# Kernel tuning notes

Hardware: AMD Instinct MI355X
Metric: run time of the kernel (lower is better)

## Reference

```python
import jax, jax.numpy as jnp
import numpy as np

B, N, D, S = 128, 1024, 512, 64
ITERS = 3
EPS = 1e-8


def setup_inputs() -> dict:
    key = jax.random.key(0)
    ks = jax.random.split(key, 10)
    inp = {
        "inputs_pe": jax.random.normal(ks[0], (B, N, D), dtype=jnp.float32),
        "inputs": jax.random.normal(ks[1], (B, N, D), dtype=jnp.float32),
        "slots": jax.random.normal(ks[2], (1, S, D), dtype=jnp.float32),
        "W1": jax.random.normal(ks[3], (D, D), dtype=jnp.float32) * 0.02,
        "b1": jnp.zeros((D,), dtype=jnp.float32),
        "W2": jax.random.normal(ks[4], (D, D), dtype=jnp.float32) * 0.02,
        "b2": jnp.zeros((D,), dtype=jnp.float32),
        "W3": jax.random.normal(ks[5], (D, D), dtype=jnp.float32) * 0.02,
        "b3": jnp.zeros((D,), dtype=jnp.float32),
    }
    return inp


def reference(inputs_pe, inputs, slots, W1, b1, W2, b2, W3, b3):
    b = inputs_pe.shape[0]
    scale = D ** (-0.5)
    # to_k: Linear -> ReLU -> Linear -> ReLU -> Linear (torch Linear: x @ W.T + b)
    h = jax.nn.relu(jnp.einsum('bnd,ed->bne', inputs_pe, W1) + b1)
    h = jax.nn.relu(jnp.einsum('bnd,ed->bne', h, W2) + b2)
    k = jnp.einsum('bnd,ed->bne', h, W3) + b3  # [b, n, d]

    q = jnp.broadcast_to(slots, (b, S, D))  # slots never updated in the loop
    for _ in range(ITERS):
        dots = jnp.einsum('bid,bjd->bij', q, k) * scale  # [b, S, n]
        s_j = dots.sum(axis=2, keepdims=True)            # sum over keys j -> [b, S, 1]
        s_all = dots.sum(axis=(1, 2), keepdims=True)     # total per batch -> [b, 1, 1]
        dots = dots / s_j * s_all
        attn = jax.nn.sigmoid(dots)
        attn2 = attn / (attn.sum(axis=-1, keepdims=True) + EPS)
        updates = jnp.einsum('bjd,bij->bid', inputs, attn2)  # [b, S, d]
    return updates, attn
```

## Files before the change

kernel.cpp:

```cpp
#include <hip/hip_runtime.h>
#include <stdint.h>

#define Bb 128
#define Nn 1024
#define Dd 512
#define Ss 64

constexpr float kScale = 0.044194173824159216f;
constexpr float kEps = 1e-8f;

typedef __bf16 bf16x8 __attribute__((ext_vector_type(8)));
typedef float f32x4 __attribute__((ext_vector_type(4)));
typedef float f32x16 __attribute__((ext_vector_type(16)));
typedef unsigned short ushort8 __attribute__((ext_vector_type(8)));

#define MFMA32 __builtin_amdgcn_mfma_f32_32x32x16_bf16

__device__ inline unsigned short f2bf_rne(float x) {
  unsigned u = __builtin_bit_cast(unsigned, x);
  u += 0x7FFFu + ((u >> 16) & 1u);
  return (unsigned short)(u >> 16);
}
__device__ inline float bf2f(unsigned short h) {
  unsigned u = ((unsigned)h) << 16;
  return __builtin_bit_cast(float, u);
}

__device__ inline void gl_lds16(const void* g, void* l) {
  typedef unsigned int u32;
  auto gp = (u32 __attribute__((address_space(1)))*)(unsigned long long)(uintptr_t)g;
  auto lp = (u32 __attribute__((address_space(3)))*)(unsigned int)(uintptr_t)l;
  __builtin_amdgcn_global_load_lds(gp, lp, 16, 0, 0);
}

__global__ void cast_split_i(const float* __restrict__ in,
                             unsigned short* __restrict__ out, int n8) {
  int i = blockIdx.x * blockDim.x + threadIdx.x;
  const int stride = gridDim.x * blockDim.x;
  for (; i < n8; i += stride) {
    const float4 v0 = ((const float4*)in)[i * 2];
    const float4 v1 = ((const float4*)in)[i * 2 + 1];
    float f[8] = {v0.x, v0.y, v0.z, v0.w, v1.x, v1.y, v1.z, v1.w};
    ushort8 h, lo;
#pragma unroll
    for (int j = 0; j < 8; j++) {
      h[j] = f2bf_rne(f[j]);
      lo[j] = f2bf_rne(f[j] - bf2f(h[j]));
    }
    ((ushort8*)out)[i * 2] = h;
    ((ushort8*)out)[i * 2 + 1] = lo;
  }
}

template <int ACT>
__global__ __launch_bounds__(512, 1) void gemm_g2(
    const unsigned short* __restrict__ A, const unsigned short* __restrict__ W,
    const float* __restrict__ bias, unsigned short* __restrict__ C) {
  constexpr int NS = 16;
  extern __shared__ unsigned short lds[];
  const int t = threadIdx.x, l = t & 63, w = t >> 6;
  const int wr = w >> 2, wc = w & 3;

  const int wg = ((blockIdx.x & 7) << 7) + (blockIdx.x >> 3);
  const long rowA0 = (long)(wg >> 1) * 256;
  const int colB0 = (wg & 1) * 256;

  const unsigned short* base8 = (w < 4) ? A + rowA0 * 1024 : W + (long)colB0 * 1024;
  const int qs = (l & 7) ^ ((l >> 3) & 7);
  const unsigned short* srcp[8];
  int dstp[8];
#pragma unroll
  for (int j = 0; j < 8; j++) {
    const int cl = (w & 3) * 8 + j;
    const int row = cl * 8 + (l >> 3);
    srcp[j] = base8 + (long)row * 1024 + qs * 8;
    dstp[j] = (w < 4 ? 0 : 16384) + cl * 512;
  }
#define STG(s)                                                            \
  {                                                                       \
    unsigned short* bq_ = lds + ((s) & 1) * 32768;                        \
    _Pragma("unroll") for (int j = 0; j < 8; j++)                         \
        gl_lds16(srcp[j] + (s) * 64, bq_ + dstp[j]);                      \
  }

  const int p0 = ((2 * (l >> 5)) ^ (l & 7)) * 8;
  int aoff[4], boff[2];
#pragma unroll
  for (int m = 0; m < 4; m++) aoff[m] = (wr * 128 + m * 32 + (l & 31)) * 64 + p0;
#pragma unroll
  for (int n = 0; n < 2; n++) boff[n] = 16384 + (wc * 64 + n * 32 + (l & 31)) * 64 + p0;

  f32x16 acc[4][2] = {};
  bf16x8 ah[4], al[4], bh0, bl0, bh1, bl1;

#define PH()                                                              \
  __builtin_amdgcn_s_barrier();                                           \
  asm volatile("s_waitcnt lgkmcnt(0)" ::: "memory");                      \
  __builtin_amdgcn_sched_barrier(0);

#define M6(MI, BH, BL, NI)                                                \
  __builtin_amdgcn_s_setprio(1);                                          \
  acc[MI][NI] = MFMA32(ah[MI], BH, acc[MI][NI], 0, 0, 0);                 \
  acc[MI][NI] = MFMA32(al[MI], BH, acc[MI][NI], 0, 0, 0);                 \
  acc[MI][NI] = MFMA32(ah[MI], BL, acc[MI][NI], 0, 0, 0);                 \
  acc[MI + 1][NI] = MFMA32(ah[MI + 1], BH, acc[MI + 1][NI], 0, 0, 0);     \
  acc[MI + 1][NI] = MFMA32(al[MI + 1], BH, acc[MI + 1][NI], 0, 0, 0);     \
  acc[MI + 1][NI] = MFMA32(ah[MI + 1], BL, acc[MI + 1][NI], 0, 0, 0);     \
  __builtin_amdgcn_s_setprio(0);                                          \
  __builtin_amdgcn_sched_barrier(0);

  STG(0);

  for (int s = 0; s < NS; ++s) {
    asm volatile("s_waitcnt vmcnt(0)" ::: "memory");
    __builtin_amdgcn_s_barrier();
    __builtin_amdgcn_sched_barrier(0);
    if (s + 1 < NS) STG(s + 1);
    const unsigned short* bq = lds + (s & 1) * 32768;

    ah[0] = *(const bf16x8*)(bq + aoff[0]);
    al[0] = *(const bf16x8*)(bq + (aoff[0] ^ 8));
    ah[1] = *(const bf16x8*)(bq + aoff[1]);
    al[1] = *(const bf16x8*)(bq + (aoff[1] ^ 8));
    bh0 = *(const bf16x8*)(bq + boff[0]);
    bl0 = *(const bf16x8*)(bq + (boff[0] ^ 8));
    PH()
    M6(0, bh0, bl0, 0)
    ah[2] = *(const bf16x8*)(bq + aoff[2]);
    al[2] = *(const bf16x8*)(bq + (aoff[2] ^ 8));
    ah[3] = *(const bf16x8*)(bq + aoff[3]);
    al[3] = *(const bf16x8*)(bq + (aoff[3] ^ 8));
    PH()
    M6(2, bh0, bl0, 0)
    bh1 = *(const bf16x8*)(bq + boff[1]);
    bl1 = *(const bf16x8*)(bq + (boff[1] ^ 8));
    PH()
    M6(0, bh1, bl1, 1)
    ah[0] = *(const bf16x8*)(bq + (aoff[0] ^ 32));
    al[0] = *(const bf16x8*)(bq + (aoff[0] ^ 40));
    ah[1] = *(const bf16x8*)(bq + (aoff[1] ^ 32));
    al[1] = *(const bf16x8*)(bq + (aoff[1] ^ 40));
    bh0 = *(const bf16x8*)(bq + (boff[0] ^ 32));
    bl0 = *(const bf16x8*)(bq + (boff[0] ^ 40));
    PH()
    M6(2, bh1, bl1, 1)
    ah[2] = *(const bf16x8*)(bq + (aoff[2] ^ 32));
    al[2] = *(const bf16x8*)(bq + (aoff[2] ^ 40));
    ah[3] = *(const bf16x8*)(bq + (aoff[3] ^ 32));
    al[3] = *(const bf16x8*)(bq + (aoff[3] ^ 40));
    PH()
    M6(0, bh0, bl0, 0)
    bh1 = *(const bf16x8*)(bq + (boff[1] ^ 32));
    bl1 = *(const bf16x8*)(bq + (boff[1] ^ 40));
    PH()
    M6(2, bh0, bl0, 0)
    PH()
    M6(0, bh1, bl1, 1)
    M6(2, bh1, bl1, 1)
  }
#undef STG
#undef PH
#undef M6

#pragma unroll
  for (int m = 0; m < 4; m++)
#pragma unroll
    for (int n = 0; n < 2; n++) {
      const int col = colB0 + wc * 64 + n * 32 + (l & 31);
      const float bv = bias[col];
      const int cofs = (col >> 3) * 16 + (col & 7);
#pragma unroll
      for (int r = 0; r < 16; r++) {
        const long row = rowA0 + wr * 128 + m * 32 + (r & 3) + 8 * (r >> 2) + 4 * (l >> 5);
        float xv = acc[m][n][r] + bv;
        if (ACT) xv = fmaxf(xv, 0.0f);
        const unsigned short h = f2bf_rne(xv);
        unsigned short* cp = C + row * 1024 + cofs;
        cp[0] = h;
        cp[8] = f2bf_rne(xv - bf2f(h));
      }
    }
}

__global__ __launch_bounds__(256) void gemm_dots_split(
    const unsigned short* __restrict__ QI, const unsigned short* __restrict__ KI,
    float* __restrict__ dots) {
  constexpr int K = 512, BM = 64, BN = 128, BK = 32;
  __shared__ __align__(16) unsigned short lah[BM * BK];
  __shared__ __align__(16) unsigned short lal[BM * BK];
  __shared__ __align__(16) unsigned short lbh[BN * BK];
  __shared__ __align__(16) unsigned short lbl[BN * BK];
  const int t = threadIdx.x, l = t & 63, w = t >> 6;
  const int b = blockIdx.x >> 3, bc = blockIdx.x & 7;
  const unsigned short* kb = KI + (long)b * Nn * 1024;
  f32x4 acc[4][2] = {};

  const int qbase = (t >> 2) * 1024 + (t & 3) * 16;
  const long kbase0 = (long)(bc * BN + (t >> 2)) * 1024 + (t & 3) * 16;
  const long kbase1 = (long)(bc * BN + 64 + (t >> 2)) * 1024 + (t & 3) * 16;

  for (int k0 = 0; k0 < K; k0 += BK) {
    const int ko = k0 * 2;
    const int lo = w * 512;
    gl_lds16(QI + qbase + ko, lah + lo);
    gl_lds16(QI + qbase + ko + 8, lal + lo);
    gl_lds16(kb + kbase0 + ko, lbh + lo);
    gl_lds16(kb + kbase0 + ko + 8, lbl + lo);
    gl_lds16(kb + kbase1 + ko, lbh + 2048 + lo);
    gl_lds16(kb + kbase1 + ko + 8, lbl + 2048 + lo);
    __syncthreads();
    bf16x8 ah[4], al[4], bh[2], bl[2];
#pragma unroll
    for (int m = 0; m < 4; m++) {
      const int off = (m * 16 + (l & 15)) * BK + (l >> 4) * 8;
      ah[m] = *(const bf16x8*)(lah + off);
      al[m] = *(const bf16x8*)(lal + off);
    }
#pragma unroll
    for (int n = 0; n < 2; n++) {
      const int off = (w * 32 + n * 16 + (l & 15)) * BK + (l >> 4) * 8;
      bh[n] = *(const bf16x8*)(lbh + off);
      bl[n] = *(const bf16x8*)(lbl + off);
    }
#pragma unroll
    for (int m = 0; m < 4; m++)
#pragma unroll
      for (int n = 0; n < 2; n++) {
        acc[m][n] = __builtin_amdgcn_mfma_f32_16x16x32_bf16(ah[m], bh[n], acc[m][n], 0, 0, 0);
        acc[m][n] = __builtin_amdgcn_mfma_f32_16x16x32_bf16(al[m], bh[n], acc[m][n], 0, 0, 0);
        acc[m][n] = __builtin_amdgcn_mfma_f32_16x16x32_bf16(ah[m], bl[n], acc[m][n], 0, 0, 0);
      }
    __syncthreads();
  }
  float* dp = dots + (long)b * Ss * Nn;
#pragma unroll
  for (int m = 0; m < 4; m++) {
    const int row = m * 16 + (l >> 4) * 4;
#pragma unroll
    for (int n = 0; n < 2; n++) {
      const int col = bc * BN + w * 32 + n * 16 + (l & 15);
#pragma unroll
      for (int r = 0; r < 4; r++) dp[(long)(row + r) * Nn + col] = acc[m][n][r] * kScale;
    }
  }
}

__global__ __launch_bounds__(256) void reduce_k(
    const float* __restrict__ dots, float* __restrict__ s_j, float* __restrict__ s_all) {
  const int b = blockIdx.x, t = threadIdx.x, l = t & 63, w = t >> 6;
  const float4* dp = (const float4*)(dots + (long)b * Ss * Nn);
  __shared__ float rowacc[64][4];
  __shared__ float rowsum[64];
  for (int r = 0; r < 64; ++r) {
    const float4 v = dp[r * 256 + t];
    float s = v.x + v.y + v.z + v.w;
#pragma unroll
    for (int off = 32; off; off >>= 1) s += __shfl_down(s, off);
    if (l == 0) rowacc[r][w] = s;
  }
  __syncthreads();
  if (t < 64) {
    const float v = rowacc[t][0] + rowacc[t][1] + rowacc[t][2] + rowacc[t][3];
    rowsum[t] = v;
    s_j[b * 64 + t] = v;
  }
  __syncthreads();
  if (t < 64) {
    float v = rowsum[t];
#pragma unroll
    for (int off = 32; off; off >>= 1) v += __shfl_down(v, off);
    if (t == 0) s_all[b] = v;
  }
}

__global__ __launch_bounds__(256) void attn_k(
    const float* __restrict__ dots, const float* __restrict__ s_j,
    const float* __restrict__ s_all, float* __restrict__ attn_out,
    float* __restrict__ inv_r) {
  const int bi = blockIdx.x;
  const int b = bi >> 6;
  const int t = threadIdx.x;
  const float ratio = s_all[b] / s_j[bi];
  const float* dp = dots + (long)bi * Nn;
  float* ap = attn_out + (long)bi * Nn;
  float s = 0.f;
#pragma unroll
  for (int qq = 0; qq < 4; qq++) {
    const int j = qq * 256 + t;
    const float x = dp[j] * ratio;
    const float a = 1.f / (1.f + expf(-x));
    ap[j] = a;
    s += a;
  }
  __shared__ float red[256];
  red[t] = s;
  __syncthreads();
  for (int off = 128; off > 0; off >>= 1) {
    if (t < off) red[t] += red[t + off];
    __syncthreads();
  }
  if (t == 0) inv_r[bi] = 1.f / (red[0] + kEps);
}

__global__ __launch_bounds__(256) void updates_k6(
    const float* __restrict__ attn, const float* __restrict__ inputs,
    const float* __restrict__ inv_r, float* __restrict__ out0) {
  constexpr int NT2 = 32;
  constexpr int BUF_F = 6144;
  extern __shared__ float ldsf[];
  const int t = threadIdx.x, l = t & 63, w = t >> 6;
  const int b = blockIdx.x >> 2, dt = blockIdx.x & 3;
  const int ig = t >> 5, dg = t & 31;
  const float* inb = inputs + (size_t)b * (Nn * Dd) + dt * 128;
  const float* attsrc = attn + (size_t)b * (Ss * Nn) + (size_t)(t >> 2) * Nn + (t & 3) * 8;
  float acc[8][4] = {};
  float4 ga0, ga1, gb0, gb1;

#define UISSUE(bufi, tile, G0, G1)                                        \
  {                                                                       \
    const int j0_ = (tile)*32;                                            \
    G0 = *(const float4*)(attsrc + j0_);                                  \
    G1 = *(const float4*)(attsrc + j0_ + 4);                              \
    float* db_ = ldsf + (bufi)*BUF_F;                                     \
    _Pragma("unroll") for (int i_ = 0; i_ < 4; i_++) {                    \
      const int row_ = i_ * 8 + w * 2 + (l >> 5);                         \
      gl_lds16(inb + (size_t)(j0_ + row_) * Dd + (l & 31) * 4,            \
               db_ + (i_ * 8 + w * 2) * 128);                             \
    }                                                                     \
  }

#define UWRITE(bufi, G0, G1)                                              \
  {                                                                       \
    float* ab_ = ldsf + (bufi)*BUF_F + 4096;                              \
    const int col_ = t >> 2;                                              \
    const int r0_ = (t & 3) * 8;                                          \
    ab_[(r0_ + 0) * 64 + col_] = G0.x;                                    \
    ab_[(r0_ + 1) * 64 + col_] = G0.y;                                    \
    ab_[(r0_ + 2) * 64 + col_] = G0.z;                                    \
    ab_[(r0_ + 3) * 64 + col_] = G0.w;                                    \
    ab_[(r0_ + 4) * 64 + col_] = G1.x;                                    \
    ab_[(r0_ + 5) * 64 + col_] = G1.y;                                    \
    ab_[(r0_ + 6) * 64 + col_] = G1.z;                                    \
    ab_[(r0_ + 7) * 64 + col_] = G1.w;                                    \
  }

#define UCOMP(bufi)                                                       \
  {                                                                       \
    const float* db_ = ldsf + (bufi)*BUF_F;                               \
    const float* ab_ = db_ + 4096;                                        \
    _Pragma("unroll 4") for (int jj = 0; jj < 32; jj++) {                 \
      float av[8];                                                        \
      float4 vv;                                                          \
      *(float4*)&av[0] = *(const float4*)(ab_ + jj * 64 + ig * 8);        \
      *(float4*)&av[4] = *(const float4*)(ab_ + jj * 64 + ig * 8 + 4);    \
      vv = *(const float4*)(db_ + jj * 128 + dg * 4);                     \
      _Pragma("unroll") for (int m_ = 0; m_ < 8; m_++) {                  \
        acc[m_][0] = __builtin_fmaf(av[m_], vv.x, acc[m_][0]);            \
        acc[m_][1] = __builtin_fmaf(av[m_], vv.y, acc[m_][1]);            \
        acc[m_][2] = __builtin_fmaf(av[m_], vv.z, acc[m_][2]);            \
        acc[m_][3] = __builtin_fmaf(av[m_], vv.w, acc[m_][3]);            \
      }                                                                   \
    }                                                                     \
  }

  UISSUE(0, 0, ga0, ga1);
  UISSUE(1, 1, gb0, gb1);
  UWRITE(0, ga0, ga1);

  for (int tt = 0; tt < NT2; tt += 2) {
    asm volatile("s_waitcnt vmcnt(6)" ::: "memory");
    UWRITE((tt + 1) % 3, gb0, gb1);
    asm volatile("s_waitcnt lgkmcnt(0)" ::: "memory");
    __builtin_amdgcn_s_barrier();
    __builtin_amdgcn_sched_barrier(0);
    if (tt < NT2 - 2) UISSUE((tt + 2) % 3, tt + 2, ga0, ga1);
    UCOMP(tt % 3);
    if (tt + 1 < NT2 - 1) {
      asm volatile("s_waitcnt vmcnt(6)" ::: "memory");
    } else {
      asm volatile("s_waitcnt vmcnt(0)" ::: "memory");
    }
    if (tt + 1 < NT2 - 1) UWRITE((tt + 2) % 3, ga0, ga1);
    asm volatile("s_waitcnt lgkmcnt(0)" ::: "memory");
    __builtin_amdgcn_s_barrier();
    __builtin_amdgcn_sched_barrier(0);
    if (tt + 1 < NT2 - 2) UISSUE((tt + 3) % 3, tt + 3, gb0, gb1);
    UCOMP((tt + 1) % 3);
  }
#undef UISSUE
#undef UWRITE
#undef UCOMP

#pragma unroll
  for (int m = 0; m < 8; m++) {
    const int i = ig * 8 + m;
    const float ir = inv_r[b * 64 + i];
    float4 o;
    o.x = acc[m][0] * ir; o.y = acc[m][1] * ir; o.z = acc[m][2] * ir; o.w = acc[m][3] * ir;
    float* op = out0 + (size_t)(b * 64 + i) * Dd + dt * 128 + dg * 4;
    *(float4*)op = o;
  }
}

extern "C" void kernel_launch(void* const* d_in, const int* in_sizes, int n_in,
                              void* d_out, int out_size, void* d_ws, size_t ws_size,
                              hipStream_t stream) {
  (void)in_sizes; (void)n_in; (void)out_size; (void)ws_size;
  const float* inputs_pe = (const float*)d_in[0];
  const float* inputs = (const float*)d_in[1];
  const float* slots = (const float*)d_in[2];
  const float* W1 = (const float*)d_in[3];
  const float* b1 = (const float*)d_in[4];
  const float* W2 = (const float*)d_in[5];
  const float* b2 = (const float*)d_in[6];
  const float* W3 = (const float*)d_in[7];
  const float* b3 = (const float*)d_in[8];

  char* ws = (char*)d_ws;
  size_t off = 0;
  auto alloc = [&](size_t bytes) -> void* {
    void* p = ws + off;
    off += (bytes + 255) & ~(size_t)255;
    return p;
  };
  const size_t actB = (size_t)Bb * Nn * 1024 * 2;
  unsigned short* AI = (unsigned short*)alloc(actB);
  unsigned short* BI = (unsigned short*)alloc(actB);
  unsigned short* w1i = (unsigned short*)alloc(Dd * 1024 * 2);
  unsigned short* w2i = (unsigned short*)alloc(Dd * 1024 * 2);
  unsigned short* w3i = (unsigned short*)alloc(Dd * 1024 * 2);
  unsigned short* qi = (unsigned short*)alloc(Ss * 1024 * 2);
  float* dotsb = (float*)alloc((size_t)Bb * Ss * Nn * 4);
  float* s_j = (float*)alloc(Bb * Ss * 4);
  float* s_all = (float*)alloc(Bb * 4);
  float* inv_r = (float*)alloc(Bb * Ss * 4);

  float* out_updates = (float*)d_out;
  float* out_attn = out_updates + (size_t)Bb * Ss * Dd;

  const int kLdsG = 2 * 64 * 1024;
  const int kLdsU = 3 * 24 * 1024;
  hipFuncSetAttribute(reinterpret_cast<const void*>(gemm_g2<1>),
                      hipFuncAttributeMaxDynamicSharedMemorySize, kLdsG);
  hipFuncSetAttribute(reinterpret_cast<const void*>(gemm_g2<0>),
                      hipFuncAttributeMaxDynamicSharedMemorySize, kLdsG);
  hipFuncSetAttribute(reinterpret_cast<const void*>(updates_k6),
                      hipFuncAttributeMaxDynamicSharedMemorySize, kLdsU);

  cast_split_i<<<4096, 256, 0, stream>>>(inputs_pe, AI, Bb * Nn * Dd / 8);
  cast_split_i<<<128, 256, 0, stream>>>(W1, w1i, Dd * Dd / 8);
  cast_split_i<<<128, 256, 0, stream>>>(W2, w2i, Dd * Dd / 8);
  cast_split_i<<<128, 256, 0, stream>>>(W3, w3i, Dd * Dd / 8);
  cast_split_i<<<16, 256, 0, stream>>>(slots, qi, Ss * Dd / 8);

  gemm_g2<1><<<1024, 512, kLdsG, stream>>>(AI, w1i, b1, BI);
  gemm_g2<1><<<1024, 512, kLdsG, stream>>>(BI, w2i, b2, AI);
  gemm_g2<0><<<1024, 512, kLdsG, stream>>>(AI, w3i, b3, BI);

  gemm_dots_split<<<Bb * 8, 256, 0, stream>>>(qi, BI, dotsb);
  reduce_k<<<Bb, 256, 0, stream>>>(dotsb, s_j, s_all);
  attn_k<<<Bb * Ss, 256, 0, stream>>>(dotsb, s_j, s_all, out_attn, inv_r);
  updates_k6<<<Bb * 4, 256, kLdsU, stream>>>(out_attn, inputs, inv_r, out_updates);
}
```

Measured before the change: 1.022 ms.

## Double-buffer dots GEMM loads and fuse row-sum reduction with sigmoid attention

The dots GEMM now uses a two-slot dynamic LDS buffer, so the next K-tile's global-to-LDS copies are issued while the current tile runs on the MFMAs, with one barrier per step instead of two. The separate reduce and attention kernels are merged into one kernel per batch. It computes row sums and the total, then applies sigmoid and per-row normalisation in a second pass, which removes a launch and the s_j and s_all intermediates. In exchange the fused kernel runs only 128 blocks, which may underuse the GPU compared with the old 8192-block attention launch, and the dots kernel uses more LDS.

Result: slower. 1.056 ms (+3.4%).

```diff
diff --git a/kernel.cpp b/kernel.cpp
--- a/kernel.cpp
+++ b/kernel.cpp
@@ -182,45 +182,56 @@
     }
 }
 
-__global__ __launch_bounds__(256) void gemm_dots_split(
+__global__ __launch_bounds__(256) void gemm_dots2(
     const unsigned short* __restrict__ QI, const unsigned short* __restrict__ KI,
     float* __restrict__ dots) {
-  constexpr int K = 512, BM = 64, BN = 128, BK = 32;
-  __shared__ __align__(16) unsigned short lah[BM * BK];
-  __shared__ __align__(16) unsigned short lal[BM * BK];
-  __shared__ __align__(16) unsigned short lbh[BN * BK];
-  __shared__ __align__(16) unsigned short lbl[BN * BK];
+  constexpr int NS = 16;
+  constexpr int SLOT = 12288;
+  extern __shared__ unsigned short ldsd[];
   const int t = threadIdx.x, l = t & 63, w = t >> 6;
   const int b = blockIdx.x >> 3, bc = blockIdx.x & 7;
   const unsigned short* kb = KI + (long)b * Nn * 1024;
   f32x4 acc[4][2] = {};
 
   const int qbase = (t >> 2) * 1024 + (t & 3) * 16;
-  const long kbase0 = (long)(bc * BN + (t >> 2)) * 1024 + (t & 3) * 16;
-  const long kbase1 = (long)(bc * BN + 64 + (t >> 2)) * 1024 + (t & 3) * 16;
-
-  for (int k0 = 0; k0 < K; k0 += BK) {
-    const int ko = k0 * 2;
-    const int lo = w * 512;
-    gl_lds16(QI + qbase + ko, lah + lo);
-    gl_lds16(QI + qbase + ko + 8, lal + lo);
-    gl_lds16(kb + kbase0 + ko, lbh + lo);
-    gl_lds16(kb + kbase0 + ko + 8, lbl + lo);
-    gl_lds16(kb + kbase1 + ko, lbh + 2048 + lo);
-    gl_lds16(kb + kbase1 + ko + 8, lbl + 2048 + lo);
-    __syncthreads();
+  const long kbase0 = (long)(bc * 128 + (t >> 2)) * 1024 + (t & 3) * 16;
+  const long kbase1 = (long)(bc * 128 + 64 + (t >> 2)) * 1024 + (t & 3) * 16;
+  const int lo = w * 512;
+
+#define DSTG(s)                                                           \
+  {                                                                       \
+    unsigned short* bq_ = ldsd + ((s) & 1) * SLOT;                        \
+    const int ko_ = (s) * 64;                                             \
+    gl_lds16(QI + qbase + ko_, bq_ + lo);                                 \
+    gl_lds16(QI + qbase + ko_ + 8, bq_ + 2048 + lo);                      \
+    gl_lds16(kb + kbase0 + ko_, bq_ + 4096 + lo);                         \
+    gl_lds16(kb + kbase0 + ko_ + 8, bq_ + 8192 + lo);                     \
+    gl_lds16(kb + kbase1 + ko_, bq_ + 4096 + 2048 + lo);                  \
+    gl_lds16(kb + kbase1 + ko_ + 8, bq_ + 8192 + 2048 + lo);              \
+  }
+
+  DSTG(0);
+
+  for (int s = 0; s < NS; ++s) {
+    asm volatile("s_waitcnt lgkmcnt(0)" ::: "memory");
+    asm volatile("s_waitcnt vmcnt(0)" ::: "memory");
+    __builtin_amdgcn_s_barrier();
+    __builtin_amdgcn_sched_barrier(0);
+    if (s + 1 < NS) DSTG(s + 1);
+    const unsigned short* bq = ldsd + (s & 1) * SLOT;
+
     bf16x8 ah[4], al[4], bh[2], bl[2];
 #pragma unroll
     for (int m = 0; m < 4; m++) {
-      const int off = (m * 16 + (l & 15)) * BK + (l >> 4) * 8;
-      ah[m] = *(const bf16x8*)(lah + off);
-      al[m] = *(const bf16x8*)(lal + off);
+      const int off = (m * 16 + (l & 15)) * 32 + (l >> 4) * 8;
+      ah[m] = *(const bf16x8*)(bq + off);
+      al[m] = *(const bf16x8*)(bq + 2048 + off);
     }
 #pragma unroll
     for (int n = 0; n < 2; n++) {
-      const int off = (w * 32 + n * 16 + (l & 15)) * BK + (l >> 4) * 8;
-      bh[n] = *(const bf16x8*)(lbh + off);
-      bl[n] = *(const bf16x8*)(lbl + off);
+      const int off = (w * 32 + n * 16 + (l & 15)) * 32 + (l >> 4) * 8;
+      bh[n] = *(const bf16x8*)(bq + 4096 + off);
+      bl[n] = *(const bf16x8*)(bq + 8192 + off);
     }
 #pragma unroll
     for (int m = 0; m < 4; m++)
@@ -230,27 +241,31 @@
         acc[m][n] = __builtin_amdgcn_mfma_f32_16x16x32_bf16(al[m], bh[n], acc[m][n], 0, 0, 0);
         acc[m][n] = __builtin_amdgcn_mfma_f32_16x16x32_bf16(ah[m], bl[n], acc[m][n], 0, 0, 0);
       }
-    __syncthreads();
-  }
+  }
+#undef DSTG
+
   float* dp = dots + (long)b * Ss * Nn;
 #pragma unroll
   for (int m = 0; m < 4; m++) {
     const int row = m * 16 + (l >> 4) * 4;
 #pragma unroll
     for (int n = 0; n < 2; n++) {
-      const int col = bc * BN + w * 32 + n * 16 + (l & 15);
+      const int col = bc * 128 + w * 32 + n * 16 + (l & 15);
 #pragma unroll
       for (int r = 0; r < 4; r++) dp[(long)(row + r) * Nn + col] = acc[m][n][r] * kScale;
     }
   }
 }
 
-__global__ __launch_bounds__(256) void reduce_k(
-    const float* __restrict__ dots, float* __restrict__ s_j, float* __restrict__ s_all) {
+__global__ __launch_bounds__(256) void reduce_attn(
+    const float* __restrict__ dots, float* __restrict__ attn_out,
+    float* __restrict__ inv_r) {
   const int b = blockIdx.x, t = threadIdx.x, l = t & 63, w = t >> 6;
   const float4* dp = (const float4*)(dots + (long)b * Ss * Nn);
+  float4* ap = (float4*)(attn_out + (long)b * Ss * Nn);
   __shared__ float rowacc[64][4];
-  __shared__ float rowsum[64];
+  __shared__ float ratio_s[64];
+  __shared__ float tot_s;
   for (int r = 0; r < 64; ++r) {
     const float4 v = dp[r * 256 + t];
     float s = v.x + v.y + v.z + v.w;
@@ -259,47 +274,34 @@
     if (l == 0) rowacc[r][w] = s;
   }
   __syncthreads();
-  if (t < 64) {
-    const float v = rowacc[t][0] + rowacc[t][1] + rowacc[t][2] + rowacc[t][3];
-    rowsum[t] = v;
-    s_j[b * 64 + t] = v;
-  }
+  if (t < 64) ratio_s[t] = rowacc[t][0] + rowacc[t][1] + rowacc[t][2] + rowacc[t][3];
   __syncthreads();
-  if (t < 64) {
-    float v = rowsum[t];
-#pragma unroll
-    for (int off = 32; off; off >>= 1) v += __shfl_down(v, off);
-    if (t == 0) s_all[b] = v;
-  }
-}
-
-__global__ __launch_bounds__(256) void attn_k(
-    const float* __restrict__ dots, const float* __restrict__ s_j,
-    const float* __restrict__ s_all, float* __restrict__ attn_out,
-    float* __restrict__ inv_r) {
-  const int bi = blockIdx.x;
-  const int b = bi >> 6;
-  const int t = threadIdx.x;
-  const float ratio = s_all[b] / s_j[bi];
-  const float* dp = dots + (long)bi * Nn;
-  float* ap = attn_out + (long)bi * Nn;
-  float s = 0.f;
-#pragma unroll
-  for (int qq = 0; qq < 4; qq++) {
-    const int j = qq * 256 + t;
-    const float x = dp[j] * ratio;
-    const float a = 1.f / (1.f + expf(-x));
-    ap[j] = a;
-    s += a;
-  }
-  __shared__ float red[256];
-  red[t] = s;
+  if (t == 0) {
+    float tot = 0.f;
+    for (int k = 0; k < 64; k++) tot += ratio_s[k];
+    tot_s = tot;
+  }
   __syncthreads();
-  for (int off = 128; off > 0; off >>= 1) {
-    if (t < off) red[t] += red[t + off];
-    __syncthreads();
-  }
-  if (t == 0) inv_r[bi] = 1.f / (red[0] + kEps);
+  if (t < 64) ratio_s[t] = tot_s / ratio_s[t];
+  __syncthreads();
+  for (int r = 0; r < 64; ++r) {
+    const float ratio = ratio_s[r];
+    const float4 v = dp[r * 256 + t];
+    float4 a;
+    a.x = 1.f / (1.f + expf(-v.x * ratio));
+    a.y = 1.f / (1.f + expf(-v.y * ratio));
+    a.z = 1.f / (1.f + expf(-v.z * ratio));
+    a.w = 1.f / (1.f + expf(-v.w * ratio));
+    ap[r * 256 + t] = a;
+    float s = a.x + a.y + a.z + a.w;
+#pragma unroll
+    for (int off = 32; off; off >>= 1) s += __shfl_down(s, off);
+    if (l == 0) rowacc[r][w] = s;
+  }
+  __syncthreads();
+  if (t < 64)
+    inv_r[b * 64 + t] =
+        1.f / (rowacc[t][0] + rowacc[t][1] + rowacc[t][2] + rowacc[t][3] + kEps);
 }
 
 __global__ __launch_bounds__(256) void updates_k6(
@@ -431,19 +433,20 @@
   unsigned short* w3i = (unsigned short*)alloc(Dd * 1024 * 2);
   unsigned short* qi = (unsigned short*)alloc(Ss * 1024 * 2);
   float* dotsb = (float*)alloc((size_t)Bb * Ss * Nn * 4);
-  float* s_j = (float*)alloc(Bb * Ss * 4);
-  float* s_all = (float*)alloc(Bb * 4);
   float* inv_r = (float*)alloc(Bb * Ss * 4);
 
   float* out_updates = (float*)d_out;
   float* out_attn = out_updates + (size_t)Bb * Ss * Dd;
 
   const int kLdsG = 2 * 64 * 1024;
+  const int kLdsD = 2 * 24 * 1024;
   const int kLdsU = 3 * 24 * 1024;
   hipFuncSetAttribute(reinterpret_cast<const void*>(gemm_g2<1>),
                       hipFuncAttributeMaxDynamicSharedMemorySize, kLdsG);
   hipFuncSetAttribute(reinterpret_cast<const void*>(gemm_g2<0>),
                       hipFuncAttributeMaxDynamicSharedMemorySize, kLdsG);
+  hipFuncSetAttribute(reinterpret_cast<const void*>(gemm_dots2),
+                      hipFuncAttributeMaxDynamicSharedMemorySize, kLdsD);
   hipFuncSetAttribute(reinterpret_cast<const void*>(updates_k6),
                       hipFuncAttributeMaxDynamicSharedMemorySize, kLdsU);
 
@@ -457,8 +460,7 @@
   gemm_g2<1><<<1024, 512, kLdsG, stream>>>(BI, w2i, b2, AI);
   gemm_g2<0><<<1024, 512, kLdsG, stream>>>(AI, w3i, b3, BI);
 
-  gemm_dots_split<<<Bb * 8, 256, 0, stream>>>(qi, BI, dotsb);
-  reduce_k<<<Bb, 256, 0, stream>>>(dotsb, s_j, s_all);
-  attn_k<<<Bb * Ss, 256, 0, stream>>>(dotsb, s_j, s_all, out_attn, inv_r);
+  gemm_dots2<<<Bb * 8, 256, kLdsD, stream>>>(qi, BI, dotsb);
+  reduce_attn<<<Bb, 256, 0, stream>>>(dotsb, out_attn, inv_r);
   updates_k6<<<Bb * 4, 256, kLdsU, stream>>>(out_attn, inputs, inv_r, out_updates);
 }
```
